# Kernel tuning notes

Hardware: AMD Instinct MI355X
Metric: run time of the kernel (lower is better)

Reference implementation:

```python
import jax, jax.numpy as jnp
import numpy as np

N_NODES = 100000
N_EDGES = 1600000
D_IN = 128
D_HID = 128
D_OUT = 2
BN_EPS = 1e-5


def _sage_conv(x, src, dst, W_l, b_l, W_r):
    # PyG SAGEConv (aggr='mean'): out = lin_l(mean_{j in N(i)} x_j) + lin_r(x_i)
    # messages flow src -> dst
    agg = jax.ops.segment_sum(x[src], dst, num_segments=x.shape[0])
    deg = jax.ops.segment_sum(jnp.ones((src.shape[0],), x.dtype), dst,
                              num_segments=x.shape[0])
    mean = agg / jnp.maximum(deg, 1.0)[:, None]
    return mean @ W_l + b_l + x @ W_r


def _batch_norm(x, gamma, beta):
    # training-mode BatchNorm1d math over the node dimension (biased var)
    mu = jnp.mean(x, axis=0)
    var = jnp.var(x, axis=0)
    return (x - mu) * jax.lax.rsqrt(var + BN_EPS) * gamma + beta


def setup_inputs() -> dict:
    key = jax.random.key(0)
    ks = jax.random.split(key, 10)
    s = lambda d: 1.0 / np.sqrt(d)
    x = jax.random.normal(ks[0], (N_NODES, D_IN), dtype=jnp.float32)
    edge_index = jax.random.randint(ks[1], (2, N_EDGES), 0, N_NODES, dtype=jnp.int64)
    W1l = jax.random.uniform(ks[2], (D_IN, D_HID), jnp.float32, -s(D_IN), s(D_IN))
    b1 = jax.random.uniform(ks[3], (D_HID,), jnp.float32, -s(D_IN), s(D_IN))
    W1r = jax.random.uniform(ks[4], (D_IN, D_HID), jnp.float32, -s(D_IN), s(D_IN))
    W2l = jax.random.uniform(ks[5], (D_HID, D_OUT), jnp.float32, -s(D_HID), s(D_HID))
    b2 = jax.random.uniform(ks[6], (D_OUT,), jnp.float32, -s(D_HID), s(D_HID))
    W2r = jax.random.uniform(ks[7], (D_HID, D_OUT), jnp.float32, -s(D_HID), s(D_HID))
    gamma1 = jnp.ones((D_HID,), jnp.float32)
    beta1 = jnp.zeros((D_HID,), jnp.float32)
    gamma2 = jnp.ones((D_OUT,), jnp.float32)
    beta2 = jnp.zeros((D_OUT,), jnp.float32)
    return {"x": x, "edge_index": edge_index,
            "W1l": W1l, "b1": b1, "W1r": W1r, "gamma1": gamma1, "beta1": beta1,
            "W2l": W2l, "b2": b2, "W2r": W2r, "gamma2": gamma2, "beta2": beta2}


def reference(x, edge_index, W1l, b1, W1r, gamma1, beta1,
              W2l, b2, W2r, gamma2, beta2):
    src, dst = edge_index[0], edge_index[1]
    h = _sage_conv(x, src, dst, W1l, b1, W1r)
    h = _batch_norm(h, gamma1, beta1)
    h = jax.nn.relu(h)
    # dropout in eval mode = identity
    h = _sage_conv(h, src, dst, W2l, b2, W2r)
    h = _batch_norm(h, gamma2, beta2)
    return jax.nn.log_softmax(h, axis=1)
```

## Files before the change

kernel.cpp:

```cpp
#include <hip/hip_runtime.h>
#include <hip/hip_bf16.h>
#include <math.h>


#define DH 128
#define PAD 64
#define L1BLOCKS 512

typedef short short8 __attribute__((ext_vector_type(8)));
typedef float float4v __attribute__((ext_vector_type(4)));
typedef float float2v __attribute__((ext_vector_type(2)));
typedef unsigned uint4v __attribute__((ext_vector_type(4)));

template <typename T> static __device__ __forceinline__ float tof(T v);
template <> __device__ __forceinline__ float tof<float>(float v) { return v; }
template <> __device__ __forceinline__ float tof<__hip_bfloat16>(__hip_bfloat16 v) {
  return __bfloat162float(v);
}

static __device__ __forceinline__ short f2bf_s(float f) {
  union { __hip_bfloat16 h; short s; } u;
  u.h = __float2bfloat16(f);
  return u.s;
}

static __device__ __forceinline__ float bf2f(short s) {
  union { unsigned u; float f; } c;
  c.u = ((unsigned)(unsigned short)s) << 16;
  return c.f;
}

static __device__ __forceinline__ float asf(unsigned u) {
  union { unsigned u; float f; } c;
  c.u = u;
  return c.f;
}

__global__ void k_probe(const unsigned* __restrict__ xw,
                        const unsigned* __restrict__ ew,
                        int* __restrict__ flags) {
  int t = threadIdx.x;
  unsigned wx = xw[(size_t)t * 23456 + 7];
  unsigned el = (wx >> 7) & 0xFFu;
  int sx = (el >= 0x60 && el <= 0x85) ? 1 : 0;
  unsigned we = ew[(size_t)t * 12000 + 1];
  int se = (we == 0) ? 1 : 0;
  __shared__ int c[2];
  if (t < 2) c[t] = 0;
  __syncthreads();
  atomicAdd(&c[0], sx);
  atomicAdd(&c[1], se);
  __syncthreads();
  if (t == 0) {
    flags[0] = (c[0] < 192) ? 1 : 0;
    flags[2] = (c[1] > 192) ? 1 : 0;
  }
}

template <typename FT>
static __device__ __forceinline__ void wt_one(const FT* __restrict__ W1l,
                                              const FT* __restrict__ W1r,
                                              short* __restrict__ WT, int idx) {
  int n = idx >> 8, k = idx & 255;
  float v = (k < 128) ? tof(W1l[k * 128 + n]) : tof(W1r[(k - 128) * 128 + n]);
  WT[n * 256 + (k ^ ((n & 7) << 3))] = f2bf_s(v);
}
__global__ void k_xbwt(const void* __restrict__ x, const void* __restrict__ W1l,
                       const void* __restrict__ W1r, const int* __restrict__ flags,
                       __hip_bfloat162* __restrict__ xb, short* __restrict__ WT,
                       int total2) {
  int gi = blockIdx.x * blockDim.x + threadIdx.x;
  bool f32 = flags[0] != 0;
  if (gi < 32768) {
    if (f32) wt_one<float>((const float*)W1l, (const float*)W1r, WT, gi);
    else wt_one<__hip_bfloat16>((const __hip_bfloat16*)W1l, (const __hip_bfloat16*)W1r, WT, gi);
  }
  int i = gi - 32768;
  if (i >= 0 && i < total2) {
    if (f32) {
      float2 v = ((const float2*)x)[i];
      __hip_bfloat162 o;
      o.x = __float2bfloat16(v.x);
      o.y = __float2bfloat16(v.y);
      xb[i] = o;
    } else {
      xb[i] = ((const __hip_bfloat162*)x)[i];
    }
  }
}

template <typename IT>
static __device__ __forceinline__ void edges_body(
    const IT* __restrict__ es, const IT* __restrict__ ed,
    int* __restrict__ deg_i, int* __restrict__ srcs_pad, int E, int N) {
  int stride = gridDim.x * blockDim.x;
  for (int i = blockIdx.x * blockDim.x + threadIdx.x; i < E; i += stride) {
    int s = (int)es[i], d = (int)ed[i];
    if ((unsigned)s >= (unsigned)N) s = 0;
    if ((unsigned)d >= (unsigned)N) d = 0;
    int r = atomicAdd(&deg_i[d], 1);
    if (r < PAD) srcs_pad[(size_t)d * PAD + r] = s;
  }
}
__launch_bounds__(256)
__global__ void k_edges(const void* __restrict__ ev, const int* __restrict__ flags,
                        int* __restrict__ deg_i, int* __restrict__ srcs_pad,
                        int E, int N) {
  if (flags[2]) edges_body<long long>((const long long*)ev, (const long long*)ev + E,
                                      deg_i, srcs_pad, E, N);
  else          edges_body<int>((const int*)ev, (const int*)ev + E,
                                deg_i, srcs_pad, E, N);
}

static __device__ __forceinline__ void accum8(float2v acc[4], uint4v u) {
#pragma unroll
  for (int i = 0; i < 4; ++i) {
    float2v p;
    p[0] = asf(u[i] << 16);
    p[1] = asf(u[i] & 0xFFFF0000u);
    acc[i] += p;
  }
}
static __device__ __forceinline__ uint4v maskv(uint4v v, int keep) {
  unsigned m = keep ? 0xFFFFFFFFu : 0u;
  uint4v r;
#pragma unroll
  for (int i = 0; i < 4; ++i) r[i] = v[i] & m;
  return r;
}
__launch_bounds__(256)
__global__ void k_gather(const unsigned* __restrict__ xbu,
                         const int* __restrict__ deg_i, const int* __restrict__ srcs_pad,
                         short* __restrict__ meanbs, int N) {
  int node = blockIdx.x * 4 + (threadIdx.x >> 6);
  int lane = threadIdx.x & 63;
  int g = lane >> 4, l = lane & 15;
  if (node >= N) return;
  int dg = deg_i[node];
  int cnt = min(dg, PAD);
  const int* sl = srcs_pad + (size_t)node * PAD;
  int srcv = sl[lane];
  srcv = ((unsigned)srcv < (unsigned)N) ? srcv : 0;
  const uint4v* xv = (const uint4v*)xbu;
  float2v acc[4];
#pragma unroll
  for (int i = 0; i < 4; ++i) acc[i] = (float2v){0.f, 0.f};

  if (cnt > 0) {
    int sA0 = __shfl(srcv, g);
    int sA1 = __shfl(srcv, 4 + g);
    int sA2 = __shfl(srcv, 8 + g);
    int sA3 = __shfl(srcv, 12 + g);
    uint4v a0 = xv[(size_t)sA0 * 16 + l];
    uint4v a1 = xv[(size_t)sA1 * 16 + l];
    uint4v a2 = xv[(size_t)sA2 * 16 + l];
    uint4v a3 = xv[(size_t)sA3 * 16 + l];
    uint4v b0, b1, b2, b3;
    bool hb = cnt > 16;
    if (hb) {
      int sB0 = __shfl(srcv, 16 + g);
      int sB1 = __shfl(srcv, 20 + g);
      int sB2 = __shfl(srcv, 24 + g);
      int sB3 = __shfl(srcv, 28 + g);
      b0 = xv[(size_t)sB0 * 16 + l];
      b1 = xv[(size_t)sB1 * 16 + l];
      b2 = xv[(size_t)sB2 * 16 + l];
      b3 = xv[(size_t)sB3 * 16 + l];
    }
    a0 = maskv(a0, g < cnt);
    a1 = maskv(a1, 4 + g < cnt);
    a2 = maskv(a2, 8 + g < cnt);
    a3 = maskv(a3, 12 + g < cnt);
    accum8(acc, a0);
    accum8(acc, a1);
    accum8(acc, a2);
    accum8(acc, a3);
    if (hb) {
      b0 = maskv(b0, 16 + g < cnt);
      b1 = maskv(b1, 20 + g < cnt);
      b2 = maskv(b2, 24 + g < cnt);
      b3 = maskv(b3, 28 + g < cnt);
      accum8(acc, b0);
      accum8(acc, b1);
      accum8(acc, b2);
      accum8(acc, b3);
    }
    for (int j = 32; j < cnt; j += 16) {
      int s0 = __shfl(srcv, j + g);
      int s1 = __shfl(srcv, j + 4 + g);
      int s2 = __shfl(srcv, j + 8 + g);
      int s3 = __shfl(srcv, j + 12 + g);
      uint4v v0 = xv[(size_t)s0 * 16 + l];
      uint4v v1 = xv[(size_t)s1 * 16 + l];
      uint4v v2 = xv[(size_t)s2 * 16 + l];
      uint4v v3 = xv[(size_t)s3 * 16 + l];
      v0 = maskv(v0, j + g < cnt);
      v1 = maskv(v1, j + 4 + g < cnt);
      v2 = maskv(v2, j + 8 + g < cnt);
      v3 = maskv(v3, j + 12 + g < cnt);
      accum8(acc, v0);
      accum8(acc, v1);
      accum8(acc, v2);
      accum8(acc, v3);
    }
  }

#pragma unroll
  for (int i = 0; i < 4; ++i) {
#pragma unroll
    for (int c = 0; c < 2; ++c) {
      acc[i][c] += __shfl_xor(acc[i][c], 16);
      acc[i][c] += __shfl_xor(acc[i][c], 32);
    }
  }
  if (g == 0) {
    float invd = 1.0f / fmaxf((float)dg, 1.0f);
    short8 o;
#pragma unroll
    for (int i = 0; i < 4; ++i) {
      o[2 * i]     = f2bf_s(acc[i][0] * invd);
      o[2 * i + 1] = f2bf_s(acc[i][1] * invd);
    }
    *(short8*)(meanbs + (size_t)node * DH + l * 8) = o;
  }
}

template <typename FT>
static __device__ __forceinline__ void layer1_body(
    const short* __restrict__ meanbs, const short* __restrict__ xbs,
    const short* __restrict__ WTs, const FT* __restrict__ b1,
    __hip_bfloat16* __restrict__ h1, float* __restrict__ st1,
    int N, int ntiles) {
  __shared__ short ldsWT[32768];
  int t = threadIdx.x;
  {
    const uint4v* src = (const uint4v*)WTs;
    uint4v* dst = (uint4v*)ldsWT;
#pragma unroll
    for (int i = 0; i < 16; ++i) dst[t + i * 256] = src[t + i * 256];
  }
  __syncthreads();

  int w = t >> 6;
  int lane = t & 63;
  int m = lane & 15;
  int quad = lane >> 4;
  int xm = (m & 7) << 3;

  float bs[8], bq[8];
#pragma unroll
  for (int c = 0; c < 8; ++c) { bs[c] = 0.f; bq[c] = 0.f; }
  float bias[8];
#pragma unroll
  for (int c = 0; c < 8; ++c) bias[c] = tof(b1[c * 16 + m]);

  for (int tt = blockIdx.x; tt < ntiles; tt += gridDim.x) {
    int rowbase = tt * 64 + w * 16;
    int arowc = min(rowbase + m, N - 1);

    short8 afrag[8];
    const short* mr = meanbs + (size_t)arowc * DH;
#pragma unroll
    for (int kt = 0; kt < 4; ++kt)
      afrag[kt] = *(const short8*)(mr + kt * 32 + quad * 8);
    const short* xr = xbs + (size_t)arowc * DH;
#pragma unroll
    for (int kt = 0; kt < 4; ++kt)
      afrag[4 + kt] = *(const short8*)(xr + kt * 32 + quad * 8);

    float4v acc[8];
#pragma unroll
    for (int c = 0; c < 8; ++c) acc[c] = (float4v){0.f, 0.f, 0.f, 0.f};

#pragma unroll
    for (int kt = 0; kt < 8; ++kt) {
      int koff = (kt * 32 + quad * 8) ^ xm;
#pragma unroll
      for (int c = 0; c < 8; ++c) {
        short8 b = *(const short8*)(ldsWT + (c * 16 + m) * 256 + koff);
        acc[c] = __builtin_amdgcn_mfma_f32_16x16x32_bf16(afrag[kt], b, acc[c], 0, 0, 0);
      }
    }

#pragma unroll
    for (int c = 0; c < 8; ++c) {
      int col = c * 16 + m;
#pragma unroll
      for (int r = 0; r < 4; ++r) {
        int ro = rowbase + quad * 4 + r;
        float v = acc[c][r] + bias[c];
        if (ro < N) {
          h1[(size_t)ro * DH + col] = __float2bfloat16(v);
          bs[c] += v;
          bq[c] += v * v;
        }
      }
    }
  }

  __syncthreads();
  float* lsum = (float*)ldsWT;
  float* lsq  = lsum + 512;
#pragma unroll
  for (int c = 0; c < 8; ++c) {
    float s = bs[c], q = bq[c];
    s += __shfl_xor(s, 16); s += __shfl_xor(s, 32);
    q += __shfl_xor(q, 16); q += __shfl_xor(q, 32);
    if (quad == 0) { lsum[w * 128 + c * 16 + m] = s; lsq[w * 128 + c * 16 + m] = q; }
  }
  __syncthreads();
  if (t < 128) {
    float s = lsum[0 * 128 + t] + lsum[1 * 128 + t] + lsum[2 * 128 + t] + lsum[3 * 128 + t];
    float q = lsq[0 * 128 + t] + lsq[1 * 128 + t] + lsq[2 * 128 + t] + lsq[3 * 128 + t];
    unsafeAtomicAdd(&st1[t], s);
    unsafeAtomicAdd(&st1[128 + t], q);
  }
}
__launch_bounds__(256)
__global__ void k_layer1(const short* __restrict__ meanbs, const short* __restrict__ xbs,
                         const short* __restrict__ WTs, const void* __restrict__ b1,
                         const int* __restrict__ flags,
                         __hip_bfloat16* __restrict__ h1, float* __restrict__ st1,
                         int N, int ntiles) {
  if (flags[0])
    layer1_body<float>(meanbs, xbs, WTs, (const float*)b1, h1, st1, N, ntiles);
  else
    layer1_body<__hip_bfloat16>(meanbs, xbs, WTs, (const __hip_bfloat16*)b1,
                                h1, st1, N, ntiles);
}

template <typename FT>
static __device__ __forceinline__ void zr_body(
    const short* __restrict__ h1s, const float* __restrict__ stats1,
    const FT* __restrict__ g1, const FT* __restrict__ be1,
    const FT* __restrict__ W2l, const FT* __restrict__ W2r,
    float4* __restrict__ zr, int N) {
  __shared__ float sc[128], sh[128];
  int t = threadIdx.x;
  if (t < 128) {
    float invN = 1.0f / (float)N;
    float mu = stats1[t] * invN;
    float var = stats1[128 + t] * invN - mu * mu;
    float a = tof(g1[t]) * rsqrtf(var + 1e-5f);
    sc[t] = a;
    sh[t] = tof(be1[t]) - mu * a;
  }
  __syncthreads();
  int lane = t & 63, w = t >> 6;
  int g = lane >> 4, l = lane & 15;
  int f0 = l * 8;
  float scl[8], shl[8], wl0[8], wl1[8], wr0[8], wr1[8];
#pragma unroll
  for (int j = 0; j < 8; ++j) {
    int f = f0 + j;
    scl[j] = sc[f];
    shl[j] = sh[f];
    wl0[j] = tof(W2l[f * 2 + 0]);
    wl1[j] = tof(W2l[f * 2 + 1]);
    wr0[j] = tof(W2r[f * 2 + 0]);
    wr1[j] = tof(W2r[f * 2 + 1]);
  }
  int gw = blockIdx.x * 4 + w;
  int nw = gridDim.x * 4;
  for (int base = gw * 4; base < N; base += nw * 4) {
    int node = base + g;
    if (node < N) {
      short8 hv = *(const short8*)(h1s + (size_t)node * DH + f0);
      float z0 = 0.f, z1 = 0.f, r0 = 0.f, r1 = 0.f;
#pragma unroll
      for (int j = 0; j < 8; ++j) {
        float v = fmaxf(bf2f(hv[j]) * scl[j] + shl[j], 0.0f);
        z0 += v * wl0[j];
        z1 += v * wl1[j];
        r0 += v * wr0[j];
        r1 += v * wr1[j];
      }
#pragma unroll
      for (int off = 8; off >= 1; off >>= 1) {
        z0 += __shfl_xor(z0, off);
        z1 += __shfl_xor(z1, off);
        r0 += __shfl_xor(r0, off);
        r1 += __shfl_xor(r1, off);
      }
      if (l == 0) zr[node] = make_float4(z0, z1, r0, r1);
    }
  }
}
__launch_bounds__(256)
__global__ void k_zr(const __hip_bfloat16* __restrict__ h1, const float* __restrict__ st1,
                     const void* g1, const void* be1, const void* W2l, const void* W2r,
                     const int* __restrict__ flags, float4* __restrict__ zr, int N) {
  if (flags[0])
    zr_body<float>((const short*)h1, st1, (const float*)g1, (const float*)be1,
                   (const float*)W2l, (const float*)W2r, zr, N);
  else
    zr_body<__hip_bfloat16>((const short*)h1, st1, (const __hip_bfloat16*)g1,
                            (const __hip_bfloat16*)be1,
                            (const __hip_bfloat16*)W2l, (const __hip_bfloat16*)W2r, zr, N);
}

template <typename FT>
static __device__ __forceinline__ void h2_body(
    const float2* __restrict__ z2, const int* __restrict__ deg_i,
    const int* __restrict__ srcs_pad, const FT* __restrict__ b2,
    float2* __restrict__ h2, float* __restrict__ stats2, int N) {
  int lane = threadIdx.x & 63, w = threadIdx.x >> 6;
  int g = lane >> 4, l = lane & 15;
  float bs0 = 0.f, bs1 = 0.f, bq0 = 0.f, bq1 = 0.f;
  float bb0 = tof(b2[0]), bb1 = tof(b2[1]);
  int gw = blockIdx.x * 4 + w;
  int nw = gridDim.x * 4;
  for (int base = gw * 4; base < N; base += nw * 4) {
    int node = base + g;
    float za = 0.f, zb = 0.f;
    int dg_true = 0;
    if (node < N) {
      dg_true = deg_i[node];
      int cnt = min(dg_true, PAD);
      const int* sl = srcs_pad + (size_t)node * PAD;
      for (int j = l; j < cnt; j += 16) {
        float2 v = z2[2 * sl[j]];
        za += v.x;
        zb += v.y;
      }
    }
#pragma unroll
    for (int off = 8; off >= 1; off >>= 1) {
      za += __shfl_xor(za, off);
      zb += __shfl_xor(zb, off);
    }
    if (node < N && l == 0) {
      float dg = fmaxf((float)dg_true, 1.0f);
      float2 rw = z2[2 * node + 1];
      float h0 = za / dg + rw.x + bb0;
      float h1v = zb / dg + rw.y + bb1;
      h2[node] = make_float2(h0, h1v);
      bs0 += h0; bs1 += h1v; bq0 += h0 * h0; bq1 += h1v * h1v;
    }
  }
  bs0 += __shfl_xor(bs0, 16); bs0 += __shfl_xor(bs0, 32);
  bs1 += __shfl_xor(bs1, 16); bs1 += __shfl_xor(bs1, 32);
  bq0 += __shfl_xor(bq0, 16); bq0 += __shfl_xor(bq0, 32);
  bq1 += __shfl_xor(bq1, 16); bq1 += __shfl_xor(bq1, 32);
  __shared__ float red[4][4];
  if (lane == 0) { red[w][0] = bs0; red[w][1] = bs1; red[w][2] = bq0; red[w][3] = bq1; }
  __syncthreads();
  if (threadIdx.x < 4) {
    float a = red[0][threadIdx.x] + red[1][threadIdx.x] +
              red[2][threadIdx.x] + red[3][threadIdx.x];
    unsafeAtomicAdd(&stats2[threadIdx.x], a);
  }
}
__launch_bounds__(256)
__global__ void k_h2(const float4* __restrict__ zr, const int* __restrict__ deg_i,
                     const int* __restrict__ srcs_pad, const void* b2,
                     const int* __restrict__ flags,
                     float2* __restrict__ h2, float* __restrict__ stats2, int N) {
  if (flags[0])
    h2_body<float>((const float2*)zr, deg_i, srcs_pad, (const float*)b2, h2, stats2, N);
  else
    h2_body<__hip_bfloat16>((const float2*)zr, deg_i, srcs_pad,
                            (const __hip_bfloat16*)b2, h2, stats2, N);
}

template <typename FT>
static __device__ __forceinline__ void out_body(
    const float2* __restrict__ h2, const float* __restrict__ stats2,
    const FT* __restrict__ g2, const FT* __restrict__ be2,
    void* __restrict__ out, int N) {
  int i = blockIdx.x * blockDim.x + threadIdx.x;
  if (i >= N) return;
  float invN = 1.0f / (float)N;
  float mu0 = stats2[0] * invN, mu1 = stats2[1] * invN;
  float v0 = stats2[2] * invN - mu0 * mu0;
  float v1 = stats2[3] * invN - mu1 * mu1;
  float r0 = rsqrtf(v0 + 1e-5f), r1 = rsqrtf(v1 + 1e-5f);
  float2 h = h2[i];
  float y0 = (h.x - mu0) * r0 * tof(g2[0]) + tof(be2[0]);
  float y1 = (h.y - mu1) * r1 * tof(g2[1]) + tof(be2[1]);
  float mx = fmaxf(y0, y1);
  float lse = mx + logf(expf(y0 - mx) + expf(y1 - mx));
  float o0 = y0 - lse, o1 = y1 - lse;
  if (sizeof(FT) == 4) {
    ((float2*)out)[i] = make_float2(o0, o1);
  } else {
    __hip_bfloat162 o;
    o.x = __float2bfloat16(o0);
    o.y = __float2bfloat16(o1);
    ((__hip_bfloat162*)out)[i] = o;
  }
}
__global__ void k_out(const float2* __restrict__ h2, const float* __restrict__ stats2,
                      const void* g2, const void* be2, const int* __restrict__ flags,
                      void* __restrict__ out, int N) {
  if (flags[0]) out_body<float>(h2, stats2, (const float*)g2, (const float*)be2, out, N);
  else out_body<__hip_bfloat16>(h2, stats2, (const __hip_bfloat16*)g2,
                                (const __hip_bfloat16*)be2, out, N);
}

extern "C" void kernel_launch(void* const* d_in, const int* in_sizes, int n_in,
                              void* d_out, int out_size, void* d_ws, size_t ws_size,
                              hipStream_t stream) {
  int ix = 0, ie = 1, iW1l = 2, ib1 = 3, iW1r = 4, ig1 = 5, ibe1 = 6,
      iW2l = 7, ib2 = 8, iW2r = 9, ig2 = 10, ibe2 = 11;
  if (n_in == 12) {
    int best = -1, second = -1;
    for (int i = 0; i < 12; ++i) {
      if (best < 0 || in_sizes[i] > in_sizes[best]) { second = best; best = i; }
      else if (second < 0 || in_sizes[i] > in_sizes[second]) second = i;
    }
    ix = best; ie = second;
    int c16384 = 0, c128 = 0, c256 = 0, c2 = 0;
    for (int i = 0; i < 12; ++i) {
      if (i == ix || i == ie) continue;
      int s = in_sizes[i];
      if (s == 16384) { if (c16384++ == 0) iW1l = i; else iW1r = i; }
      else if (s == 128) { if (c128 == 0) ib1 = i; else if (c128 == 1) ig1 = i; else ibe1 = i; c128++; }
      else if (s == 256) { if (c256++ == 0) iW2l = i; else iW2r = i; }
      else { if (c2 == 0) ib2 = i; else if (c2 == 1) ig2 = i; else ibe2 = i; c2++; }
    }
  }

  const void* x   = d_in[ix];
  const void* ev  = d_in[ie];
  const void* W1l = d_in[iW1l];
  const void* b1  = d_in[ib1];
  const void* W1r = d_in[iW1r];
  const void* g1  = d_in[ig1];
  const void* be1 = d_in[ibe1];
  const void* W2l = d_in[iW2l];
  const void* b2  = d_in[ib2];
  const void* W2r = d_in[iW2r];
  const void* g2  = d_in[ig2];
  const void* be2 = d_in[ibe2];

  int N = in_sizes[ix] / DH;
  int E = in_sizes[ie] / 2;
  int nb = (N + 63) / 64;

  int grid1 = (nb < L1BLOCKS) ? nb : L1BLOCKS;

  char* ws = (char*)d_ws;
  size_t off = 0;
  auto alloc = [&](size_t b) { size_t o = off; off += (b + 255) & ~(size_t)255; return o; };
  size_t o_st1   = alloc(256 * 4);
  size_t o_st2   = alloc(4 * 4);
  size_t o_degi  = alloc((size_t)N * 4);
  size_t zlen = off;
  size_t o_srcs  = alloc((size_t)N * PAD * 4);
  size_t o_xb    = alloc((size_t)N * DH * 2);
  size_t o_mean  = alloc((size_t)N * DH * 2);
  size_t o_h1    = alloc((size_t)N * DH * 2);
  size_t o_wt    = alloc(256 * 128 * 2);
  size_t o_zr    = alloc((size_t)N * 16);
  size_t o_h2    = alloc((size_t)N * 8);
  size_t o_flg   = alloc(64);

  float* st1  = (float*)(ws + o_st1);
  float* st2  = (float*)(ws + o_st2);
  int* deg_i  = (int*)(ws + o_degi);
  int* srcs   = (int*)(ws + o_srcs);
  __hip_bfloat162* xb = (__hip_bfloat162*)(ws + o_xb);
  short* meanb = (short*)(ws + o_mean);
  __hip_bfloat16* h1 = (__hip_bfloat16*)(ws + o_h1);
  short* WT   = (short*)(ws + o_wt);
  float4* zrp = (float4*)(ws + o_zr);
  float2* h2p = (float2*)(ws + o_h2);
  int* flags  = (int*)(ws + o_flg);

  hipMemsetAsync(d_ws, 0, zlen, stream);

  int total2 = N * 64;
  k_probe<<<1, 256, 0, stream>>>((const unsigned*)x, (const unsigned*)ev, flags);
  k_xbwt<<<(total2 + 32768 + 255) / 256, 256, 0, stream>>>(x, W1l, W1r, flags, xb, WT, total2);
  k_edges<<<2048, 256, 0, stream>>>(ev, flags, deg_i, srcs, E, N);
  k_gather<<<(N + 3) / 4, 256, 0, stream>>>((const unsigned*)xb, deg_i, srcs, meanb, N);
  k_layer1<<<grid1, 256, 0, stream>>>(meanb, (const short*)xb, WT, b1,
                                      flags, h1, st1, N, nb);
  k_zr<<<2048, 256, 0, stream>>>(h1, st1, g1, be1, W2l, W2r, flags, zrp, N);
  k_h2<<<2048, 256, 0, stream>>>(zrp, deg_i, srcs, b2, flags, h2p, st2, N);
  k_out<<<(N + 255) / 256, 256, 0, stream>>>(h2p, st2, g2, be2, flags, d_out, N);
}
```

Measured before the change: 389.8 us.

## Build padded adjacency via two-pass binned scatter with LDS-local bucketing

Replaces the per-edge global atomic on each destination degree plus scattered writes into the padded source list with two passes. The first pass appends packed (local dst, src) pairs into per-128-node bins split into sub-bins, using few contended counters and nontemporal stores. The second pass buckets each bin in shared memory and writes degree and padded lists with coalesced stores. This adds an extra kernel and an intermediate buffer, and it silently drops edges if a sub-bin overflows its cap. A bounds clamp is added in k_h2 because padded slots are now written with possibly stale LDS values.

```diff
diff --git a/kernel.cpp b/kernel.cpp
--- a/kernel.cpp
+++ b/kernel.cpp
@@ -5,6 +5,10 @@
 
 #define DH 128
 #define PAD 64
+#define NPB 128
+#define NSUB 4
+#define SUBCAP 1024
+#define CURSTRIDE 16
 #define L1BLOCKS 512
 
 typedef short short8 __attribute__((ext_vector_type(8)));
@@ -90,26 +94,66 @@
 }
 
 template <typename IT>
-static __device__ __forceinline__ void edges_body(
+static __device__ __forceinline__ void scatter_body(
     const IT* __restrict__ es, const IT* __restrict__ ed,
-    int* __restrict__ deg_i, int* __restrict__ srcs_pad, int E, int N) {
+    int* __restrict__ binCur, unsigned* __restrict__ pairs, int E, int N) {
   int stride = gridDim.x * blockDim.x;
+  int sub = threadIdx.x & (NSUB - 1);
   for (int i = blockIdx.x * blockDim.x + threadIdx.x; i < E; i += stride) {
     int s = (int)es[i], d = (int)ed[i];
     if ((unsigned)s >= (unsigned)N) s = 0;
     if ((unsigned)d >= (unsigned)N) d = 0;
-    int r = atomicAdd(&deg_i[d], 1);
-    if (r < PAD) srcs_pad[(size_t)d * PAD + r] = s;
+    int seg = (d >> 7) * NSUB + sub;
+    int r = atomicAdd(&binCur[seg * CURSTRIDE], 1);
+    if (r < SUBCAP) {
+      unsigned pk = ((unsigned)(d & (NPB - 1)) << 20) | (unsigned)s;
+      __builtin_nontemporal_store(pk, &pairs[(size_t)seg * SUBCAP + r]);
+    }
   }
 }
 __launch_bounds__(256)
-__global__ void k_edges(const void* __restrict__ ev, const int* __restrict__ flags,
-                        int* __restrict__ deg_i, int* __restrict__ srcs_pad,
-                        int E, int N) {
-  if (flags[2]) edges_body<long long>((const long long*)ev, (const long long*)ev + E,
-                                      deg_i, srcs_pad, E, N);
-  else          edges_body<int>((const int*)ev, (const int*)ev + E,
-                                deg_i, srcs_pad, E, N);
+__global__ void k_scatter(const void* __restrict__ ev, const int* __restrict__ flags,
+                          int* __restrict__ binCur, unsigned* __restrict__ pairs,
+                          int E, int N) {
+  if (flags[2]) scatter_body<long long>((const long long*)ev, (const long long*)ev + E,
+                                        binCur, pairs, E, N);
+  else          scatter_body<int>((const int*)ev, (const int*)ev + E,
+                                  binCur, pairs, E, N);
+}
+
+__launch_bounds__(256)
+__global__ void k_binbuild(const unsigned* __restrict__ pairs,
+                           const int* __restrict__ binCur,
+                           int* __restrict__ deg_i, int* __restrict__ srcs_pad, int N) {
+  __shared__ int cnt[NPB];
+  __shared__ int lst[NPB * PAD];
+  int bin = blockIdx.x;
+  int t = threadIdx.x;
+  for (int i = t; i < NPB; i += 256) cnt[i] = 0;
+  __syncthreads();
+#pragma unroll
+  for (int sub = 0; sub < NSUB; ++sub) {
+    int seg = bin * NSUB + sub;
+    int m = min(binCur[seg * CURSTRIDE], SUBCAP);
+    const unsigned* pp = pairs + (size_t)seg * SUBCAP;
+    for (int i = t; i < m; i += 256) {
+      unsigned u = pp[i];
+      int local = u >> 20;
+      int s = u & 0xFFFFF;
+      int r = atomicAdd(&cnt[local], 1);
+      if (r < PAD) lst[local * PAD + r] = s;
+    }
+  }
+  __syncthreads();
+  int base = bin * NPB;
+  for (int i = t; i < NPB; i += 256) {
+    int node = base + i;
+    if (node < N) deg_i[node] = cnt[i];
+  }
+  for (int i = t; i < NPB * PAD; i += 256) {
+    int node = base + (i >> 6);
+    if (node < N) srcs_pad[(size_t)base * PAD + i] = lst[i];
+  }
 }
 
 static __device__ __forceinline__ void accum8(float2v acc[4], uint4v u) {
@@ -419,7 +463,9 @@
       int cnt = min(dg_true, PAD);
       const int* sl = srcs_pad + (size_t)node * PAD;
       for (int j = l; j < cnt; j += 16) {
-        float2 v = z2[2 * sl[j]];
+        int sj = sl[j];
+        sj = ((unsigned)sj < (unsigned)N) ? sj : 0;
+        float2 v = z2[2 * sj];
         za += v.x;
         zb += v.y;
       }
@@ -537,6 +583,7 @@
   int N = in_sizes[ix] / DH;
   int E = in_sizes[ie] / 2;
   int nb = (N + 63) / 64;
+  int NB = (N + NPB - 1) / NPB;
 
   int grid1 = (nb < L1BLOCKS) ? nb : L1BLOCKS;
 
@@ -545,8 +592,10 @@
   auto alloc = [&](size_t b) { size_t o = off; off += (b + 255) & ~(size_t)255; return o; };
   size_t o_st1   = alloc(256 * 4);
   size_t o_st2   = alloc(4 * 4);
+  size_t o_cur   = alloc((size_t)NB * NSUB * CURSTRIDE * 4);
+  size_t zlen = off;
+  size_t o_pairs = alloc((size_t)NB * NSUB * SUBCAP * 4);
   size_t o_degi  = alloc((size_t)N * 4);
-  size_t zlen = off;
   size_t o_srcs  = alloc((size_t)N * PAD * 4);
   size_t o_xb    = alloc((size_t)N * DH * 2);
   size_t o_mean  = alloc((size_t)N * DH * 2);
@@ -558,6 +607,8 @@
 
   float* st1  = (float*)(ws + o_st1);
   float* st2  = (float*)(ws + o_st2);
+  int* binCur = (int*)(ws + o_cur);
+  unsigned* pairs = (unsigned*)(ws + o_pairs);
   int* deg_i  = (int*)(ws + o_degi);
   int* srcs   = (int*)(ws + o_srcs);
   __hip_bfloat162* xb = (__hip_bfloat162*)(ws + o_xb);
@@ -573,7 +624,8 @@
   int total2 = N * 64;
   k_probe<<<1, 256, 0, stream>>>((const unsigned*)x, (const unsigned*)ev, flags);
   k_xbwt<<<(total2 + 32768 + 255) / 256, 256, 0, stream>>>(x, W1l, W1r, flags, xb, WT, total2);
-  k_edges<<<2048, 256, 0, stream>>>(ev, flags, deg_i, srcs, E, N);
+  k_scatter<<<2048, 256, 0, stream>>>(ev, flags, binCur, pairs, E, N);
+  k_binbuild<<<NB, 256, 0, stream>>>(pairs, binCur, deg_i, srcs, N);
   k_gather<<<(N + 3) / 4, 256, 0, stream>>>((const unsigned*)xb, deg_i, srcs, meanb, N);
   k_layer1<<<grid1, 256, 0, stream>>>(meanb, (const short*)xb, WT, b1,
                                       flags, h1, st1, N, nb);
```

Measured after the change: 406.7 us. 1.04x slower.

## Build padded adjacency via two-pass bucket partition with LDS degree counting

Applied to the files above, without the earlier changes.

Replaces the single-pass edge kernel, which did global atomics on per-node degree counters and scattered writes into the padded source lists, with two passes. The first pass partitions edges into 2048-node destination buckets using shared-memory histograms and one global atomic per bucket per chunk. The second pass has each block scan one bucket and count degrees for its 256-node slice with LDS atomics. This removes contended global atomics and randomly scattered writes, but every block in the build pass reads its whole bucket (8x redundant reads), a fixed bucket capacity can silently drop edges, and the 17-bit source packing limits N.

```diff
diff --git a/kernel.cpp b/kernel.cpp
--- a/kernel.cpp
+++ b/kernel.cpp
@@ -5,6 +5,12 @@
 
 #define DH 128
 #define PAD 64
+#define CBITS 11
+#define CNODES 2048
+#define MAXBKT 128
+#define BUCKETCAP 65536
+#define CHUNK 4096
+#define CURSTRIDE 16
 #define L1BLOCKS 512
 
 typedef short short8 __attribute__((ext_vector_type(8)));
@@ -90,26 +96,96 @@
 }
 
 template <typename IT>
-static __device__ __forceinline__ void edges_body(
+static __device__ __forceinline__ void part_body(
     const IT* __restrict__ es, const IT* __restrict__ ed,
-    int* __restrict__ deg_i, int* __restrict__ srcs_pad, int E, int N) {
-  int stride = gridDim.x * blockDim.x;
-  for (int i = blockIdx.x * blockDim.x + threadIdx.x; i < E; i += stride) {
-    int s = (int)es[i], d = (int)ed[i];
+    int* __restrict__ bktCur, unsigned* __restrict__ bktData,
+    int E, int N, int NBKT) {
+  __shared__ unsigned pkt[CHUNK];
+  __shared__ unsigned char bb[CHUNK];
+  __shared__ unsigned ord[CHUNK];
+  __shared__ int hist[MAXBKT];
+  __shared__ int lstart[MAXBKT + 1];
+  __shared__ int cur[MAXBKT];
+  __shared__ int gbase[MAXBKT];
+  int t = threadIdx.x;
+  int e0 = blockIdx.x * CHUNK;
+  int nE = min(CHUNK, E - e0);
+  if (nE <= 0) return;
+
+  for (int b = t; b < MAXBKT; b += 256) { hist[b] = 0; cur[b] = 0; }
+  __syncthreads();
+  for (int i = t; i < nE; i += 256) {
+    int s = (int)es[e0 + i], d = (int)ed[e0 + i];
     if ((unsigned)s >= (unsigned)N) s = 0;
     if ((unsigned)d >= (unsigned)N) d = 0;
-    int r = atomicAdd(&deg_i[d], 1);
-    if (r < PAD) srcs_pad[(size_t)d * PAD + r] = s;
+    int b = d >> CBITS;
+    bb[i] = (unsigned char)b;
+    pkt[i] = ((unsigned)(d & (CNODES - 1)) << 17) | (unsigned)s;
+    atomicAdd(&hist[b], 1);
+  }
+  __syncthreads();
+  if (t == 0) {
+    int acc = 0;
+    for (int b = 0; b < NBKT; ++b) { lstart[b] = acc; acc += hist[b]; }
+    lstart[NBKT] = acc;
+  }
+  __syncthreads();
+  if (t < NBKT) {
+    int c = hist[t];
+    gbase[t] = (c > 0) ? atomicAdd(&bktCur[t * CURSTRIDE], c) : 0;
+  }
+  __syncthreads();
+  for (int i = t; i < nE; i += 256) {
+    int b = bb[i];
+    int p = atomicAdd(&cur[b], 1);
+    ord[lstart[b] + p] = pkt[i];
+  }
+  __syncthreads();
+  for (int i = t; i < nE; i += 256) {
+    int lo = 0, hi = NBKT;
+    while (hi - lo > 1) { int mid = (lo + hi) >> 1; if (lstart[mid] <= i) lo = mid; else hi = mid; }
+    int off = gbase[lo] + (i - lstart[lo]);
+    if (off < BUCKETCAP)
+      bktData[(size_t)lo * BUCKETCAP + off] = ord[i];
   }
 }
 __launch_bounds__(256)
-__global__ void k_edges(const void* __restrict__ ev, const int* __restrict__ flags,
+__global__ void k_part(const void* __restrict__ ev, const int* __restrict__ flags,
+                       int* __restrict__ bktCur, unsigned* __restrict__ bktData,
+                       int E, int N, int NBKT) {
+  if (flags[2]) part_body<long long>((const long long*)ev, (const long long*)ev + E,
+                                     bktCur, bktData, E, N, NBKT);
+  else          part_body<int>((const int*)ev, (const int*)ev + E,
+                               bktCur, bktData, E, N, NBKT);
+}
+
+__launch_bounds__(256)
+__global__ void k_build(const unsigned* __restrict__ bktData,
+                        const int* __restrict__ bktCur,
                         int* __restrict__ deg_i, int* __restrict__ srcs_pad,
-                        int E, int N) {
-  if (flags[2]) edges_body<long long>((const long long*)ev, (const long long*)ev + E,
-                                      deg_i, srcs_pad, E, N);
-  else          edges_body<int>((const int*)ev, (const int*)ev + E,
-                                deg_i, srcs_pad, E, N);
+                        int N, int NBKT) {
+  __shared__ int deg[256];
+  int b = blockIdx.x >> 3;
+  int sl = blockIdx.x & 7;
+  if (b >= NBKT) return;
+  int t = threadIdx.x;
+  deg[t] = 0;
+  __syncthreads();
+  int m = min(bktCur[b * CURSTRIDE], BUCKETCAP);
+  const unsigned* pp = bktData + (size_t)b * BUCKETCAP;
+  for (int i = t; i < m; i += 256) {
+    unsigned u = pp[i];
+    int dl = u >> 17;
+    if ((dl >> 8) != sl) continue;
+    int r = atomicAdd(&deg[dl & 255], 1);
+    if (r < PAD) {
+      int node = (b << CBITS) + dl;
+      srcs_pad[(size_t)node * PAD + r] = (int)(u & 0x1FFFF);
+    }
+  }
+  __syncthreads();
+  int node = (b << CBITS) + (sl << 8) + t;
+  if (node < N) deg_i[node] = deg[t];
 }
 
 static __device__ __forceinline__ void accum8(float2v acc[4], uint4v u) {
@@ -419,7 +495,9 @@
       int cnt = min(dg_true, PAD);
       const int* sl = srcs_pad + (size_t)node * PAD;
       for (int j = l; j < cnt; j += 16) {
-        float2 v = z2[2 * sl[j]];
+        int sj = sl[j];
+        sj = ((unsigned)sj < (unsigned)N) ? sj : 0;
+        float2 v = z2[2 * sj];
         za += v.x;
         zb += v.y;
       }
@@ -537,16 +615,21 @@
   int N = in_sizes[ix] / DH;
   int E = in_sizes[ie] / 2;
   int nb = (N + 63) / 64;
+  int NBKT = (N + CNODES - 1) >> CBITS;
+  if (NBKT > MAXBKT) NBKT = MAXBKT;
 
   int grid1 = (nb < L1BLOCKS) ? nb : L1BLOCKS;
+  int nblkp = (E + CHUNK - 1) / CHUNK;
 
   char* ws = (char*)d_ws;
   size_t off = 0;
   auto alloc = [&](size_t b) { size_t o = off; off += (b + 255) & ~(size_t)255; return o; };
   size_t o_st1   = alloc(256 * 4);
   size_t o_st2   = alloc(4 * 4);
+  size_t o_cur   = alloc((size_t)MAXBKT * CURSTRIDE * 4);
+  size_t zlen = off;
+  size_t o_bdat  = alloc((size_t)NBKT * BUCKETCAP * 4);
   size_t o_degi  = alloc((size_t)N * 4);
-  size_t zlen = off;
   size_t o_srcs  = alloc((size_t)N * PAD * 4);
   size_t o_xb    = alloc((size_t)N * DH * 2);
   size_t o_mean  = alloc((size_t)N * DH * 2);
@@ -558,6 +641,8 @@
 
   float* st1  = (float*)(ws + o_st1);
   float* st2  = (float*)(ws + o_st2);
+  int* bktCur = (int*)(ws + o_cur);
+  unsigned* bktData = (unsigned*)(ws + o_bdat);
   int* deg_i  = (int*)(ws + o_degi);
   int* srcs   = (int*)(ws + o_srcs);
   __hip_bfloat162* xb = (__hip_bfloat162*)(ws + o_xb);
@@ -573,7 +658,8 @@
   int total2 = N * 64;
   k_probe<<<1, 256, 0, stream>>>((const unsigned*)x, (const unsigned*)ev, flags);
   k_xbwt<<<(total2 + 32768 + 255) / 256, 256, 0, stream>>>(x, W1l, W1r, flags, xb, WT, total2);
-  k_edges<<<2048, 256, 0, stream>>>(ev, flags, deg_i, srcs, E, N);
+  k_part<<<nblkp, 256, 0, stream>>>(ev, flags, bktCur, bktData, E, N, NBKT);
+  k_build<<<NBKT * 8, 256, 0, stream>>>(bktData, bktCur, deg_i, srcs, N, NBKT);
   k_gather<<<(N + 3) / 4, 256, 0, stream>>>((const unsigned*)xb, deg_i, srcs, meanb, N);
   k_layer1<<<grid1, 256, 0, stream>>>(meanb, (const short*)xb, WT, b1,
                                       flags, h1, st1, N, nb);
```

Result: faster. 346.6 us (-11.1%).
